# Kernel tuning notes

Measured on AMD Instinct MI355X. Metric: run time of the kernel, lower is better.

## Reference

```python
import jax, jax.numpy as jnp
import numpy as np

N = 50000      # nodes
E = 800000     # edges (avg degree 16)
H = 4          # attention heads
F_IN = 256     # input feature dim
D = 64         # per-head hidden/out dim (hidden*H = 256 chains into next layer)
NEG_SLOPE = 0.2  # DGL GATConv default leaky_relu slope


def setup_inputs() -> dict:
    key = jax.random.key(0)
    ks = jax.random.split(key, 12)
    inp = {
        "features": jax.random.normal(ks[0], (N, F_IN), jnp.float32),
        "src": jax.random.randint(ks[1], (E,), 0, N, jnp.int32),
        "dst": jax.random.randint(ks[2], (E,), 0, N, jnp.int32),
    }
    dims = [(F_IN, D), (H * D, D), (H * D, D)]
    for i, (fin, dout) in enumerate(dims):
        sc = 1.0 / np.sqrt(fin)
        inp[f"W{i+1}"] = jax.random.normal(ks[3 + 3 * i], (fin, H * dout), jnp.float32) * sc
        inp[f"al{i+1}"] = jax.random.normal(ks[4 + 3 * i], (H, dout), jnp.float32) * 0.1
        inp[f"ar{i+1}"] = jax.random.normal(ks[5 + 3 * i], (H, dout), jnp.float32) * 0.1
        inp[f"b{i+1}"] = jnp.zeros((H * dout,), jnp.float32)
    return inp


def gat_layer(h, src, dst, W, al, ar, b, act):
    n = h.shape[0]
    feat = (h @ W).reshape(n, H, -1)                     # [N, H, D]
    el = jnp.sum(feat * al, axis=-1)                     # [N, H]
    er = jnp.sum(feat * ar, axis=-1)                     # [N, H]
    e = jax.nn.leaky_relu(el[src] + er[dst], NEG_SLOPE)  # [E, H]
    # segment (per-dst) softmax over incoming edges
    m = jax.ops.segment_max(e, dst, num_segments=n)      # [N, H]
    ex = jnp.exp(e - m[dst])
    s = jax.ops.segment_sum(ex, dst, num_segments=n)
    alpha = ex / jnp.maximum(s[dst], 1e-9)               # [E, H]
    # weighted scatter-aggregate of source features
    out = jax.ops.segment_sum(feat[src] * alpha[..., None], dst, num_segments=n)  # [N, H, D]
    out = out + b.reshape(1, H, -1)
    if act:
        out = jax.nn.elu(out)
    return out.reshape(n, -1)                            # flatten(1): concat heads


def reference(features, src, dst, W1, al1, ar1, b1, W2, al2, ar2, b2, W3, al3, ar3, b3):
    h = gat_layer(features, src, dst, W1, al1, ar1, b1, act=True)
    h = gat_layer(h, src, dst, W2, al2, ar2, b2, act=True)
    h = gat_layer(h, src, dst, W3, al3, ar3, b3, act=False)
    return h  # [N, H*D] = [50000, 256]
```

## Files before the change

### kernel.cpp

```cpp
#include <hip/hip_runtime.h>
#include <hip/hip_bf16.h>
#include <cstdint>


#define FEAT 256
#define NHEAD 4

typedef short short8 __attribute__((ext_vector_type(8)));
typedef float f32x4 __attribute__((ext_vector_type(4)));

__device__ __forceinline__ ushort f2bf(float v) {
    uint u = __float_as_uint(v);
    uint r = (u + 0x7fffu + ((u >> 16) & 1u)) >> 16;
    return (ushort)r;
}
__device__ __forceinline__ float bf2f(ushort h) {
    return __uint_as_float(((uint)h) << 16);
}

__global__ void hist_kernel(const int* __restrict__ dst, int* __restrict__ deg, int E) {
    int e = blockIdx.x * 256 + threadIdx.x;
    if (e < E) atomicAdd(&deg[dst[e]], 1);
}

__global__ void scan_block(const int* __restrict__ deg, int* __restrict__ offs,
                           int* __restrict__ bsums, int n) {
    __shared__ int s[256];
    int i = blockIdx.x * 256 + threadIdx.x;
    int v = (i < n) ? deg[i] : 0;
    s[threadIdx.x] = v; __syncthreads();
    #pragma unroll
    for (int off = 1; off < 256; off <<= 1) {
        int t = (threadIdx.x >= off) ? s[threadIdx.x - off] : 0;
        __syncthreads();
        s[threadIdx.x] += t;
        __syncthreads();
    }
    if (i < n) offs[i] = s[threadIdx.x] - v;
    if (threadIdx.x == 255) bsums[blockIdx.x] = s[255];
}

__global__ void scan_sums(int* __restrict__ bsums, int nb) {
    __shared__ int s[256];
    int v = (threadIdx.x < nb) ? bsums[threadIdx.x] : 0;
    s[threadIdx.x] = v; __syncthreads();
    #pragma unroll
    for (int off = 1; off < 256; off <<= 1) {
        int t = (threadIdx.x >= off) ? s[threadIdx.x - off] : 0;
        __syncthreads();
        s[threadIdx.x] += t;
        __syncthreads();
    }
    if (threadIdx.x < nb) bsums[threadIdx.x] = s[threadIdx.x] - v;
}

__global__ void scan_add(int* __restrict__ offs, int* __restrict__ cursor,
                         const int* __restrict__ bsums, int n, int total) {
    int i = blockIdx.x * 256 + threadIdx.x;
    if (i < n) {
        int o = offs[i] + bsums[i >> 8];
        offs[i] = o;
        cursor[i] = o;
    }
    if (i == 0) offs[n] = total;
}

__global__ void scatter_kernel(const int* __restrict__ src, const int* __restrict__ dst,
                               int* __restrict__ cursor, int* __restrict__ csr_src, int E) {
    int e = blockIdx.x * 256 + threadIdx.x;
    if (e < E) {
        int d = dst[e];
        int pos = atomicAdd(&cursor[d], 1);
        csr_src[pos] = src[e];
    }
}

__global__ void wprep3_kernel(const float* __restrict__ W0, const float* __restrict__ W1,
                              const float* __restrict__ W2,
                              ushort* __restrict__ Wh0, ushort* __restrict__ Wl0,
                              ushort* __restrict__ Wh1, ushort* __restrict__ Wl1,
                              ushort* __restrict__ Wh2, ushort* __restrict__ Wl2) {
    const float* W = (blockIdx.y == 0) ? W0 : (blockIdx.y == 1) ? W1 : W2;
    ushort* Wh = (blockIdx.y == 0) ? Wh0 : (blockIdx.y == 1) ? Wh1 : Wh2;
    ushort* Wl = (blockIdx.y == 0) ? Wl0 : (blockIdx.y == 1) ? Wl1 : Wl2;
    int n = blockIdx.x;
    int k = threadIdx.x;
    float v = W[(size_t)k * FEAT + n];
    ushort h = f2bf(v);
    float r = v - bf2f(h);
    Wh[(size_t)n * FEAT + k] = h;
    Wl[(size_t)n * FEAT + k] = f2bf(r);
}

__global__ void fsplit_kernel(const float* __restrict__ A, ushort* __restrict__ Ah,
                              ushort* __restrict__ Al, int total8) {
    int i = blockIdx.x * 256 + threadIdx.x;
    if (i >= total8) return;
    const float4* p = (const float4*)(A + (size_t)i * 8);
    float4 a = p[0], b = p[1];
    float v[8] = {a.x, a.y, a.z, a.w, b.x, b.y, b.z, b.w};
    ushort hi[8], lo[8];
    #pragma unroll
    for (int t = 0; t < 8; ++t) {
        hi[t] = f2bf(v[t]);
        lo[t] = f2bf(v[t] - bf2f(hi[t]));
    }
    *(short8*)(Ah + (size_t)i * 8) = *(short8*)hi;
    *(short8*)(Al + (size_t)i * 8) = *(short8*)lo;
}

#define GBM 64
#define GBK 32
#define LDK 40
#define NKIT (FEAT / GBK)

__global__ __launch_bounds__(256) void gemm_fused(const ushort* __restrict__ Ahg,
                                                  const ushort* __restrict__ Alg,
                                                  const ushort* __restrict__ Whg,
                                                  const ushort* __restrict__ Wlg,
                                                  const float* __restrict__ alv,
                                                  const float* __restrict__ arv,
                                                  ushort* __restrict__ featB,
                                                  float* __restrict__ el,
                                                  float* __restrict__ er, int M) {
    __shared__ ushort Ah[2][GBM][LDK];
    __shared__ ushort Al[2][GBM][LDK];

    const int tid  = threadIdx.x;
    const int lane = tid & 63;
    const int wid  = tid >> 6;
    const int row0 = blockIdx.x * GBM;

    const int arow = tid >> 2;
    const int achk = (tid & 3) * 8;
    const bool aok = (row0 + arow) < M;
    const ushort* ApH = Ahg + (size_t)(row0 + arow) * FEAT + achk;
    const ushort* ApL = Alg + (size_t)(row0 + arow) * FEAT + achk;

    const int fr = lane & 15;
    const int fk = (lane >> 4) * 8;
    const int q  = lane >> 4;

    f32x4 acc[4][4];
    #pragma unroll
    for (int i = 0; i < 4; ++i)
        #pragma unroll
        for (int j = 0; j < 4; ++j) {
            f32x4 z = {0.f, 0.f, 0.f, 0.f};
            acc[i][j] = z;
        }

    const short8 z8 = {0, 0, 0, 0, 0, 0, 0, 0};

    {
        short8 a_h = aok ? *(const short8*)(ApH) : z8;
        short8 a_l = aok ? *(const short8*)(ApL) : z8;
        *(short8*)&Ah[0][arow][achk] = a_h;
        *(short8*)&Al[0][arow][achk] = a_l;
    }

    #pragma unroll
    for (int t = 0; t < NKIT; ++t) {
        const int cur = t & 1;
        const int k0 = t * GBK;
        short8 a_h = z8, a_l = z8;
        if (t + 1 < NKIT && aok) {
            a_h = *(const short8*)(ApH + k0 + GBK);
            a_l = *(const short8*)(ApL + k0 + GBK);
        }
        short8 bfh[4], bfl[4];
        #pragma unroll
        for (int nt = 0; nt < 4; ++nt) {
            size_t boff = (size_t)(wid * 64 + nt * 16 + fr) * FEAT + k0 + fk;
            bfh[nt] = *(const short8*)(Whg + boff);
            bfl[nt] = *(const short8*)(Wlg + boff);
        }

        __syncthreads();

        #pragma unroll
        for (int mt = 0; mt < 4; ++mt) {
            short8 afh = *(const short8*)&Ah[cur][mt * 16 + fr][fk];
            short8 afl = *(const short8*)&Al[cur][mt * 16 + fr][fk];
            #pragma unroll
            for (int nt = 0; nt < 4; ++nt) {
                acc[mt][nt] = __builtin_amdgcn_mfma_f32_16x16x32_bf16(
                    afh, bfh[nt], acc[mt][nt], 0, 0, 0);
                acc[mt][nt] = __builtin_amdgcn_mfma_f32_16x16x32_bf16(
                    afh, bfl[nt], acc[mt][nt], 0, 0, 0);
                acc[mt][nt] = __builtin_amdgcn_mfma_f32_16x16x32_bf16(
                    afl, bfh[nt], acc[mt][nt], 0, 0, 0);
            }
        }
        if (t + 1 < NKIT) {
            *(short8*)&Ah[cur ^ 1][arow][achk] = a_h;
            *(short8*)&Al[cur ^ 1][arow][achk] = a_l;
        }
    }

    float al4[4], ar4[4];
    #pragma unroll
    for (int nt = 0; nt < 4; ++nt) {
        al4[nt] = alv[wid * 64 + nt * 16 + fr];
        ar4[nt] = arv[wid * 64 + nt * 16 + fr];
    }
    #pragma unroll
    for (int mt = 0; mt < 4; ++mt) {
        #pragma unroll
        for (int r = 0; r < 4; ++r) {
            int row = row0 + mt * 16 + q * 4 + r;
            bool ok = row < M;
            float pl = 0.f, pr = 0.f;
            #pragma unroll
            for (int nt = 0; nt < 4; ++nt) {
                float v = acc[mt][nt][r];
                if (ok) featB[(size_t)row * FEAT + wid * 64 + nt * 16 + fr] = f2bf(v);
                pl = fmaf(v, al4[nt], pl);
                pr = fmaf(v, ar4[nt], pr);
            }
            #pragma unroll
            for (int o = 1; o < 16; o <<= 1) {
                pl += __shfl_xor(pl, o, 64);
                pr += __shfl_xor(pr, o, 64);
            }
            if (ok && fr == 0) {
                el[(size_t)row * NHEAD + wid] = pl;
                er[(size_t)row * NHEAD + wid] = pr;
            }
        }
    }
}

__global__ __launch_bounds__(256) void agg_kernel3(const ushort* __restrict__ featB,
                                                   const float* __restrict__ el,
                                                   const float* __restrict__ er,
                                                   const int* __restrict__ offs,
                                                   const int* __restrict__ csr_src,
                                                   const float* __restrict__ bias,
                                                   float* __restrict__ outF,
                                                   ushort* __restrict__ outH,
                                                   ushort* __restrict__ outL,
                                                   int act, int n) {
    int node = blockIdx.x * 4 + (threadIdx.x >> 6);
    if (node >= n) return;
    int lane = threadIdx.x & 63;
    int h = lane >> 4;
    int j16 = lane & 15;
    int f = lane * 4;
    int start = offs[node];
    int deg = offs[node + 1] - start;
    float erh = er[node * NHEAD + h];

    float m = -1e30f, ssum = 0.f;
    float acc0 = 0.f, acc1 = 0.f, acc2 = 0.f, acc3 = 0.f;
    int sidx = (j16 < deg) ? csr_src[start + j16] : 0;

    for (int p0 = 0; p0 < deg; p0 += 16) {
        int pn = p0 + 16 + j16;
        int sidx_nx = (pn < deg) ? csr_src[start + pn] : 0;
        float e = -1e30f;
        if (p0 + j16 < deg) {
            float t = el[sidx * NHEAD + h] + erh;
            e = (t > 0.f) ? t : 0.2f * t;
        }
        float cm = e;
        #pragma unroll
        for (int o = 1; o < 16; o <<= 1) cm = fmaxf(cm, __shfl_xor(cm, o, 64));
        float newm = fmaxf(m, cm);
        float sc = __expf(m - newm);
        m = newm;
        ssum *= sc; acc0 *= sc; acc1 *= sc; acc2 *= sc; acc3 *= sc;
        float w = __expf(e - m);
        ssum += w;
        int cnt = min(16, deg - p0);
        if (cnt == 16) {
            #pragma unroll
            for (int j = 0; j < 16; ++j) {
                float wj = __shfl(w, j, 16);
                int sj = __shfl(sidx, j, 16);
                ushort4 v = *(const ushort4*)(featB + (size_t)sj * FEAT + f);
                acc0 = fmaf(wj, bf2f(v.x), acc0);
                acc1 = fmaf(wj, bf2f(v.y), acc1);
                acc2 = fmaf(wj, bf2f(v.z), acc2);
                acc3 = fmaf(wj, bf2f(v.w), acc3);
            }
        } else {
            for (int j = 0; j < cnt; ++j) {
                float wj = __shfl(w, j, 16);
                int sj = __shfl(sidx, j, 16);
                ushort4 v = *(const ushort4*)(featB + (size_t)sj * FEAT + f);
                acc0 = fmaf(wj, bf2f(v.x), acc0);
                acc1 = fmaf(wj, bf2f(v.y), acc1);
                acc2 = fmaf(wj, bf2f(v.z), acc2);
                acc3 = fmaf(wj, bf2f(v.w), acc3);
            }
        }
        sidx = sidx_nx;
    }
    float st = ssum;
    #pragma unroll
    for (int o = 1; o < 16; o <<= 1) st += __shfl_xor(st, o, 64);
    float inv = 1.f / fmaxf(st, 1e-9f);
    float4 b4 = *(const float4*)(bias + f);
    float o0 = fmaf(acc0, inv, b4.x);
    float o1 = fmaf(acc1, inv, b4.y);
    float o2 = fmaf(acc2, inv, b4.z);
    float o3 = fmaf(acc3, inv, b4.w);
    if (act) {
        o0 = (o0 > 0.f) ? o0 : expm1f(o0);
        o1 = (o1 > 0.f) ? o1 : expm1f(o1);
        o2 = (o2 > 0.f) ? o2 : expm1f(o2);
        o3 = (o3 > 0.f) ? o3 : expm1f(o3);
    }
    if (outF) {
        *((float4*)(outF + (size_t)node * FEAT + f)) = make_float4(o0, o1, o2, o3);
    } else {
        ushort4 hh, ll;
        hh.x = f2bf(o0); ll.x = f2bf(o0 - bf2f(hh.x));
        hh.y = f2bf(o1); ll.y = f2bf(o1 - bf2f(hh.y));
        hh.z = f2bf(o2); ll.z = f2bf(o2 - bf2f(hh.z));
        hh.w = f2bf(o3); ll.w = f2bf(o3 - bf2f(hh.w));
        *(ushort4*)(outH + (size_t)node * FEAT + f) = hh;
        *(ushort4*)(outL + (size_t)node * FEAT + f) = ll;
    }
}

extern "C" void kernel_launch(void* const* d_in, const int* in_sizes, int n_in,
                              void* d_out, int out_size, void* d_ws, size_t ws_size,
                              hipStream_t stream) {
    const float* features = (const float*)d_in[0];
    const int*   src      = (const int*)d_in[1];
    const int*   dst      = (const int*)d_in[2];
    const int N = in_sizes[0] / FEAT;
    const int E = in_sizes[1];

    char* ws = (char*)d_ws;
    size_t off = 0;
    auto carve = [&](size_t bytes) -> void* {
        void* p = ws + off;
        off = (off + bytes + 255) & ~(size_t)255;
        return p;
    };
    int*    deg     = (int*)carve((size_t)N * 4);
    int*    offs    = (int*)carve((size_t)(N + 1) * 4);
    int*    cursor  = (int*)carve((size_t)N * 4);
    int*    bsums   = (int*)carve(4096);
    int*    csr_src = (int*)carve((size_t)E * 4);
    float*  el      = (float*)carve((size_t)N * NHEAD * 4);
    float*  er      = (float*)carve((size_t)N * NHEAD * 4);
    ushort* featB   = (ushort*)carve((size_t)N * FEAT * 2);
    ushort* inAh    = (ushort*)carve((size_t)N * FEAT * 2);
    ushort* inAl    = (ushort*)carve((size_t)N * FEAT * 2);
    ushort* Wh[3], *Wl[3];
    for (int i = 0; i < 3; ++i) {
        Wh[i] = (ushort*)carve((size_t)FEAT * FEAT * 2);
        Wl[i] = (ushort*)carve((size_t)FEAT * FEAT * 2);
    }

    const int nbE = (E + 255) / 256;
    const int nbN = (N + 255) / 256;

    hipMemsetAsync(deg, 0, (size_t)N * 4, stream);
    hist_kernel<<<nbE, 256, 0, stream>>>(dst, deg, E);
    scan_block<<<nbN, 256, 0, stream>>>(deg, offs, bsums, N);
    scan_sums<<<1, 256, 0, stream>>>(bsums, nbN);
    scan_add<<<nbN, 256, 0, stream>>>(offs, cursor, bsums, N, E);
    scatter_kernel<<<nbE, 256, 0, stream>>>(src, dst, cursor, csr_src, E);
    dim3 wgrid(FEAT, 3);
    wprep3_kernel<<<wgrid, FEAT, 0, stream>>>((const float*)d_in[3], (const float*)d_in[7],
                                              (const float*)d_in[11],
                                              Wh[0], Wl[0], Wh[1], Wl[1], Wh[2], Wl[2]);
    const int total8 = N * FEAT / 8;
    fsplit_kernel<<<(total8 + 255) / 256, 256, 0, stream>>>(features, inAh, inAl, total8);

    const int gemmBlocks = (N + GBM - 1) / GBM;
    const int nodeBlocks = (N + 3) / 4;

    gemm_fused<<<gemmBlocks, 256, 0, stream>>>(inAh, inAl, Wh[0], Wl[0],
                                               (const float*)d_in[4], (const float*)d_in[5],
                                               featB, el, er, N);
    agg_kernel3<<<nodeBlocks, 256, 0, stream>>>(featB, el, er, offs, csr_src,
                                                (const float*)d_in[6],
                                                (float*)nullptr, inAh, inAl, 1, N);
    gemm_fused<<<gemmBlocks, 256, 0, stream>>>(inAh, inAl, Wh[1], Wl[1],
                                               (const float*)d_in[8], (const float*)d_in[9],
                                               featB, el, er, N);
    agg_kernel3<<<nodeBlocks, 256, 0, stream>>>(featB, el, er, offs, csr_src,
                                                (const float*)d_in[10],
                                                (float*)nullptr, inAh, inAl, 1, N);
    gemm_fused<<<gemmBlocks, 256, 0, stream>>>(inAh, inAl, Wh[2], Wl[2],
                                               (const float*)d_in[12], (const float*)d_in[13],
                                               featB, el, er, N);
    agg_kernel3<<<nodeBlocks, 256, 0, stream>>>(featB, el, er, offs, csr_src,
                                                (const float*)d_in[14],
                                                (float*)d_out, (ushort*)nullptr, (ushort*)nullptr, 0, N);
}
```

Baseline: 490.0 us.

## Double GEMM row tile and split aggregation gather across half-waves with 16-byte loads

The GEMM row tile grows from 64 to 128 rows per block, so each loaded W fragment feeds twice as many MFMAs; each thread now stages 16 A elements. The aggregation kernel now has each half-wave handle alternate edges, with every lane gathering 8 bf16 features in one 16-byte load. Partial sums are then combined with a cross-half shuffle and one half writes the output. The aim is fewer, wider gather instructions and better reuse of W, at the cost of more accumulator registers in the GEMM (possibly lower occupancy) and extra shuffles in the aggregation.

```diff
diff --git a/kernel.cpp b/kernel.cpp
--- a/kernel.cpp
+++ b/kernel.cpp
@@ -109,7 +109,7 @@
     *(short8*)(Al + (size_t)i * 8) = *(short8*)lo;
 }
 
-#define GBM 64
+#define GBM 128
 #define GBK 32
 #define LDK 40
 #define NKIT (FEAT / GBK)
@@ -131,8 +131,8 @@
     const int wid  = tid >> 6;
     const int row0 = blockIdx.x * GBM;
 
-    const int arow = tid >> 2;
-    const int achk = (tid & 3) * 8;
+    const int arow = tid >> 1;
+    const int achk = (tid & 1) * 16;
     const bool aok = (row0 + arow) < M;
     const ushort* ApH = Ahg + (size_t)(row0 + arow) * FEAT + achk;
     const ushort* ApL = Alg + (size_t)(row0 + arow) * FEAT + achk;
@@ -141,9 +141,9 @@
     const int fk = (lane >> 4) * 8;
     const int q  = lane >> 4;
 
-    f32x4 acc[4][4];
-    #pragma unroll
-    for (int i = 0; i < 4; ++i)
+    f32x4 acc[8][4];
+    #pragma unroll
+    for (int i = 0; i < 8; ++i)
         #pragma unroll
         for (int j = 0; j < 4; ++j) {
             f32x4 z = {0.f, 0.f, 0.f, 0.f};
@@ -153,20 +153,26 @@
     const short8 z8 = {0, 0, 0, 0, 0, 0, 0, 0};
 
     {
-        short8 a_h = aok ? *(const short8*)(ApH) : z8;
-        short8 a_l = aok ? *(const short8*)(ApL) : z8;
-        *(short8*)&Ah[0][arow][achk] = a_h;
-        *(short8*)&Al[0][arow][achk] = a_l;
+        short8 h0 = aok ? *(const short8*)(ApH)     : z8;
+        short8 h1 = aok ? *(const short8*)(ApH + 8) : z8;
+        short8 l0 = aok ? *(const short8*)(ApL)     : z8;
+        short8 l1 = aok ? *(const short8*)(ApL + 8) : z8;
+        *(short8*)&Ah[0][arow][achk]     = h0;
+        *(short8*)&Ah[0][arow][achk + 8] = h1;
+        *(short8*)&Al[0][arow][achk]     = l0;
+        *(short8*)&Al[0][arow][achk + 8] = l1;
     }
 
     #pragma unroll
     for (int t = 0; t < NKIT; ++t) {
         const int cur = t & 1;
         const int k0 = t * GBK;
-        short8 a_h = z8, a_l = z8;
+        short8 h0 = z8, h1 = z8, l0 = z8, l1 = z8;
         if (t + 1 < NKIT && aok) {
-            a_h = *(const short8*)(ApH + k0 + GBK);
-            a_l = *(const short8*)(ApL + k0 + GBK);
+            h0 = *(const short8*)(ApH + k0 + GBK);
+            h1 = *(const short8*)(ApH + k0 + GBK + 8);
+            l0 = *(const short8*)(ApL + k0 + GBK);
+            l1 = *(const short8*)(ApL + k0 + GBK + 8);
         }
         short8 bfh[4], bfl[4];
         #pragma unroll
@@ -179,7 +185,7 @@
         __syncthreads();
 
         #pragma unroll
-        for (int mt = 0; mt < 4; ++mt) {
+        for (int mt = 0; mt < 8; ++mt) {
             short8 afh = *(const short8*)&Ah[cur][mt * 16 + fr][fk];
             short8 afl = *(const short8*)&Al[cur][mt * 16 + fr][fk];
             #pragma unroll
@@ -193,8 +199,10 @@
             }
         }
         if (t + 1 < NKIT) {
-            *(short8*)&Ah[cur ^ 1][arow][achk] = a_h;
-            *(short8*)&Al[cur ^ 1][arow][achk] = a_l;
+            *(short8*)&Ah[cur ^ 1][arow][achk]     = h0;
+            *(short8*)&Ah[cur ^ 1][arow][achk + 8] = h1;
+            *(short8*)&Al[cur ^ 1][arow][achk]     = l0;
+            *(short8*)&Al[cur ^ 1][arow][achk + 8] = l1;
         }
     }
 
@@ -205,7 +213,7 @@
         ar4[nt] = arv[wid * 64 + nt * 16 + fr];
     }
     #pragma unroll
-    for (int mt = 0; mt < 4; ++mt) {
+    for (int mt = 0; mt < 8; ++mt) {
         #pragma unroll
         for (int r = 0; r < 4; ++r) {
             int row = row0 + mt * 16 + q * 4 + r;
@@ -231,7 +239,7 @@
     }
 }
 
-__global__ __launch_bounds__(256) void agg_kernel3(const ushort* __restrict__ featB,
+__global__ __launch_bounds__(256) void agg_kernel5(const ushort* __restrict__ featB,
                                                    const float* __restrict__ el,
                                                    const float* __restrict__ er,
                                                    const int* __restrict__ offs,
@@ -244,15 +252,19 @@
     int node = blockIdx.x * 4 + (threadIdx.x >> 6);
     if (node >= n) return;
     int lane = threadIdx.x & 63;
-    int h = lane >> 4;
+    int h   = lane >> 4;
     int j16 = lane & 15;
-    int f = lane * 4;
+    int l31 = lane & 31;
+    int par = lane >> 5;
+    int fb  = l31 * 8;
+    int hh  = l31 >> 3;
     int start = offs[node];
     int deg = offs[node + 1] - start;
     float erh = er[node * NHEAD + h];
 
     float m = -1e30f, ssum = 0.f;
-    float acc0 = 0.f, acc1 = 0.f, acc2 = 0.f, acc3 = 0.f;
+    float a0 = 0.f, a1 = 0.f, a2 = 0.f, a3 = 0.f;
+    float a4 = 0.f, a5 = 0.f, a6 = 0.f, a7 = 0.f;
     int sidx = (j16 < deg) ? csr_src[start + j16] : 0;
 
     for (int p0 = 0; p0 < deg; p0 += 16) {
@@ -269,59 +281,79 @@
         float newm = fmaxf(m, cm);
         float sc = __expf(m - newm);
         m = newm;
-        ssum *= sc; acc0 *= sc; acc1 *= sc; acc2 *= sc; acc3 *= sc;
+        ssum *= sc;
         float w = __expf(e - m);
         ssum += w;
+        float scA = __shfl(sc, hh * 16, 64);
+        a0 *= scA; a1 *= scA; a2 *= scA; a3 *= scA;
+        a4 *= scA; a5 *= scA; a6 *= scA; a7 *= scA;
         int cnt = min(16, deg - p0);
-        if (cnt == 16) {
+        int iters = (cnt + 1) >> 1;
+        for (int i = 0; i < iters; ++i) {
+            int j0 = 2 * i + par;
+            int sj = __shfl(sidx, j0, 16);
+            float wj = __shfl(w, hh * 16 + j0, 64);
+            short8 v = *(const short8*)(featB + (size_t)sj * FEAT + fb);
+            a0 = fmaf(wj, bf2f((ushort)v[0]), a0);
+            a1 = fmaf(wj, bf2f((ushort)v[1]), a1);
+            a2 = fmaf(wj, bf2f((ushort)v[2]), a2);
+            a3 = fmaf(wj, bf2f((ushort)v[3]), a3);
+            a4 = fmaf(wj, bf2f((ushort)v[4]), a4);
+            a5 = fmaf(wj, bf2f((ushort)v[5]), a5);
+            a6 = fmaf(wj, bf2f((ushort)v[6]), a6);
+            a7 = fmaf(wj, bf2f((ushort)v[7]), a7);
+        }
+        sidx = sidx_nx;
+    }
+    a0 += __shfl_xor(a0, 32, 64);
+    a1 += __shfl_xor(a1, 32, 64);
+    a2 += __shfl_xor(a2, 32, 64);
+    a3 += __shfl_xor(a3, 32, 64);
+    a4 += __shfl_xor(a4, 32, 64);
+    a5 += __shfl_xor(a5, 32, 64);
+    a6 += __shfl_xor(a6, 32, 64);
+    a7 += __shfl_xor(a7, 32, 64);
+
+    float st = ssum;
+    #pragma unroll
+    for (int o = 1; o < 16; o <<= 1) st += __shfl_xor(st, o, 64);
+    float stA = __shfl(st, hh * 16, 64);
+    if (par == 0) {
+        float inv = 1.f / fmaxf(stA, 1e-9f);
+        float4 b0 = *(const float4*)(bias + fb);
+        float4 b1 = *(const float4*)(bias + fb + 4);
+        float o0 = fmaf(a0, inv, b0.x);
+        float o1 = fmaf(a1, inv, b0.y);
+        float o2 = fmaf(a2, inv, b0.z);
+        float o3 = fmaf(a3, inv, b0.w);
+        float o4 = fmaf(a4, inv, b1.x);
+        float o5 = fmaf(a5, inv, b1.y);
+        float o6 = fmaf(a6, inv, b1.z);
+        float o7 = fmaf(a7, inv, b1.w);
+        if (act) {
+            o0 = (o0 > 0.f) ? o0 : expm1f(o0);
+            o1 = (o1 > 0.f) ? o1 : expm1f(o1);
+            o2 = (o2 > 0.f) ? o2 : expm1f(o2);
+            o3 = (o3 > 0.f) ? o3 : expm1f(o3);
+            o4 = (o4 > 0.f) ? o4 : expm1f(o4);
+            o5 = (o5 > 0.f) ? o5 : expm1f(o5);
+            o6 = (o6 > 0.f) ? o6 : expm1f(o6);
+            o7 = (o7 > 0.f) ? o7 : expm1f(o7);
+        }
+        if (outF) {
+            *((float4*)(outF + (size_t)node * FEAT + fb))     = make_float4(o0, o1, o2, o3);
+            *((float4*)(outF + (size_t)node * FEAT + fb + 4)) = make_float4(o4, o5, o6, o7);
+        } else {
+            ushort hi[8], lo[8];
+            float ov[8] = {o0, o1, o2, o3, o4, o5, o6, o7};
             #pragma unroll
-            for (int j = 0; j < 16; ++j) {
-                float wj = __shfl(w, j, 16);
-                int sj = __shfl(sidx, j, 16);
-                ushort4 v = *(const ushort4*)(featB + (size_t)sj * FEAT + f);
-                acc0 = fmaf(wj, bf2f(v.x), acc0);
-                acc1 = fmaf(wj, bf2f(v.y), acc1);
-                acc2 = fmaf(wj, bf2f(v.z), acc2);
-                acc3 = fmaf(wj, bf2f(v.w), acc3);
+            for (int k = 0; k < 8; ++k) {
+                hi[k] = f2bf(ov[k]);
+                lo[k] = f2bf(ov[k] - bf2f(hi[k]));
             }
-        } else {
-            for (int j = 0; j < cnt; ++j) {
-                float wj = __shfl(w, j, 16);
-                int sj = __shfl(sidx, j, 16);
-                ushort4 v = *(const ushort4*)(featB + (size_t)sj * FEAT + f);
-                acc0 = fmaf(wj, bf2f(v.x), acc0);
-                acc1 = fmaf(wj, bf2f(v.y), acc1);
-                acc2 = fmaf(wj, bf2f(v.z), acc2);
-                acc3 = fmaf(wj, bf2f(v.w), acc3);
-            }
-        }
-        sidx = sidx_nx;
-    }
-    float st = ssum;
-    #pragma unroll
-    for (int o = 1; o < 16; o <<= 1) st += __shfl_xor(st, o, 64);
-    float inv = 1.f / fmaxf(st, 1e-9f);
-    float4 b4 = *(const float4*)(bias + f);
-    float o0 = fmaf(acc0, inv, b4.x);
-    float o1 = fmaf(acc1, inv, b4.y);
-    float o2 = fmaf(acc2, inv, b4.z);
-    float o3 = fmaf(acc3, inv, b4.w);
-    if (act) {
-        o0 = (o0 > 0.f) ? o0 : expm1f(o0);
-        o1 = (o1 > 0.f) ? o1 : expm1f(o1);
-        o2 = (o2 > 0.f) ? o2 : expm1f(o2);
-        o3 = (o3 > 0.f) ? o3 : expm1f(o3);
-    }
-    if (outF) {
-        *((float4*)(outF + (size_t)node * FEAT + f)) = make_float4(o0, o1, o2, o3);
-    } else {
-        ushort4 hh, ll;
-        hh.x = f2bf(o0); ll.x = f2bf(o0 - bf2f(hh.x));
-        hh.y = f2bf(o1); ll.y = f2bf(o1 - bf2f(hh.y));
-        hh.z = f2bf(o2); ll.z = f2bf(o2 - bf2f(hh.z));
-        hh.w = f2bf(o3); ll.w = f2bf(o3 - bf2f(hh.w));
-        *(ushort4*)(outH + (size_t)node * FEAT + f) = hh;
-        *(ushort4*)(outL + (size_t)node * FEAT + f) = ll;
+            *(short8*)(outH + (size_t)node * FEAT + fb) = *(short8*)hi;
+            *(short8*)(outL + (size_t)node * FEAT + fb) = *(short8*)lo;
+        }
     }
 }
 
@@ -379,19 +411,19 @@
     gemm_fused<<<gemmBlocks, 256, 0, stream>>>(inAh, inAl, Wh[0], Wl[0],
                                                (const float*)d_in[4], (const float*)d_in[5],
                                                featB, el, er, N);
-    agg_kernel3<<<nodeBlocks, 256, 0, stream>>>(featB, el, er, offs, csr_src,
+    agg_kernel5<<<nodeBlocks, 256, 0, stream>>>(featB, el, er, offs, csr_src,
                                                 (const float*)d_in[6],
                                                 (float*)nullptr, inAh, inAl, 1, N);
     gemm_fused<<<gemmBlocks, 256, 0, stream>>>(inAh, inAl, Wh[1], Wl[1],
                                                (const float*)d_in[8], (const float*)d_in[9],
                                                featB, el, er, N);
-    agg_kernel3<<<nodeBlocks, 256, 0, stream>>>(featB, el, er, offs, csr_src,
+    agg_kernel5<<<nodeBlocks, 256, 0, stream>>>(featB, el, er, offs, csr_src,
                                                 (const float*)d_in[10],
                                                 (float*)nullptr, inAh, inAl, 1, N);
     gemm_fused<<<gemmBlocks, 256, 0, stream>>>(inAh, inAl, Wh[2], Wl[2],
                                                (const float*)d_in[12], (const float*)d_in[13],
                                                featB, el, er, N);
-    agg_kernel3<<<nodeBlocks, 256, 0, stream>>>(featB, el, er, offs, csr_src,
+    agg_kernel5<<<nodeBlocks, 256, 0, stream>>>(featB, el, er, offs, csr_src,
                                                 (const float*)d_in[14],
                                                 (float*)d_out, (ushort*)nullptr, (ushort*)nullptr, 0, N);
 }
```

New measurement: 474.0 us. -3.3%, faster.
